# Optimization experiments

Hardware: AMD Instinct MI355X
Metric: run time of the kernel (lower is better)

The kernel has to match this reference:

```python
import jax, jax.numpy as jnp
import numpy as np

N_NODES = 50000
N_EDGES = 800000
D_IN = 128
HIDDEN = 64
N_CLASSES = 2


def gcn_conv(x, edge_index, W, b, num_nodes):
    """PyG GCNConv: linear (no bias) -> add self-loops -> sym-normalized aggregate -> + bias."""
    h = x @ W  # [N, H]
    loop = jnp.arange(num_nodes, dtype=edge_index.dtype)
    src = jnp.concatenate([edge_index[0], loop])  # [E+N]
    dst = jnp.concatenate([edge_index[1], loop])
    deg = jax.ops.segment_sum(jnp.ones_like(dst, dtype=h.dtype), dst, num_segments=num_nodes)
    dinv = jnp.where(deg > 0, jax.lax.rsqrt(deg), 0.0)
    norm = dinv[src] * dinv[dst]  # [E+N]
    msg = h[src] * norm[:, None]  # [E+N, H]  (gather + scale)
    out = jax.ops.segment_sum(msg, dst, num_segments=num_nodes)  # scatter-add
    return out + b


def setup_inputs() -> dict:
    key = jax.random.key(0)
    ks = jax.random.split(key, 6)
    x = jax.random.normal(ks[0], (N_NODES, D_IN), dtype=jnp.float32)
    edge_index = jax.random.randint(ks[1], (2, N_EDGES), 0, N_NODES, dtype=jnp.int64)
    # Glorot-ish init for weights, zero bias (PyG default)
    W1 = jax.random.normal(ks[2], (D_IN, HIDDEN), dtype=jnp.float32) * (1.0 / np.sqrt(D_IN))
    b1 = jnp.zeros((HIDDEN,), dtype=jnp.float32)
    W2 = jax.random.normal(ks[3], (HIDDEN, N_CLASSES), dtype=jnp.float32) * (1.0 / np.sqrt(HIDDEN))
    b2 = jnp.zeros((N_CLASSES,), dtype=jnp.float32)
    return {"x": x, "edge_index": edge_index, "W1": W1, "b1": b1, "W2": W2, "b2": b2}


def reference(x, edge_index, W1, b1, W2, b2):
    h = jax.nn.relu(gcn_conv(x, edge_index, W1, b1, N_NODES))
    # F.dropout(training=self.training) is identity in eval mode
    out = gcn_conv(h, edge_index, W2, b2, N_NODES)
    return out
```

## Files before the change

kernel.cpp:

```cpp
#include <hip/hip_runtime.h>

#define N_NODES 50000
#define N_EDGES 800000
#define D_IN 128
#define HIDDEN 64
#define N_CLASSES 2
#define NBUK 782
#define NBLK 196
#define NE4 200000
#define XPAD 136
#define CAP 2048

typedef _Float16 half4v __attribute__((ext_vector_type(4)));
typedef _Float16 h8 __attribute__((ext_vector_type(8)));
typedef float f4 __attribute__((ext_vector_type(4)));
typedef float f8 __attribute__((ext_vector_type(8)));


__global__ __launch_bounds__(256) void k_gemm_bin(
    const int4* __restrict__ src4, const int4* __restrict__ dst4,
    int* __restrict__ cnt, int* __restrict__ ebin,
    const float* __restrict__ x, const float* __restrict__ W1,
    _Float16* __restrict__ hs)
{
    __shared__ __attribute__((aligned(16))) _Float16 smem[2 * 64 * XPAD];
    const int t = threadIdx.x;

    if (blockIdx.x < NBLK) {
        int* hist = (int*)smem;
        for (int i = t; i < NBUK; i += 256) hist[i] = 0;
        __syncthreads();
        int base4 = blockIdx.x * 1024;
        int4 dv[4], sv[4];
        bool val[4];
#pragma unroll
        for (int k = 0; k < 4; k++) {
            int idx = base4 + k * 256 + t;
            val[k] = (idx < NE4);
            if (val[k]) {
                dv[k] = dst4[idx];
                sv[k] = src4[idx];
                atomicAdd(&hist[dv[k].x >> 6], 1);
                atomicAdd(&hist[dv[k].y >> 6], 1);
                atomicAdd(&hist[dv[k].z >> 6], 1);
                atomicAdd(&hist[dv[k].w >> 6], 1);
            }
        }
        __syncthreads();
        for (int i = t; i < NBUK; i += 256) {
            int c = hist[i];
            hist[i] = c ? atomicAdd(&cnt[i], c) : 0;
        }
        __syncthreads();
#pragma unroll
        for (int k = 0; k < 4; k++) {
            if (val[k]) {
                int b0 = dv[k].x >> 6, b1 = dv[k].y >> 6;
                int b2 = dv[k].z >> 6, b3 = dv[k].w >> 6;
                int p0 = atomicAdd(&hist[b0], 1);
                int p1 = atomicAdd(&hist[b1], 1);
                int p2 = atomicAdd(&hist[b2], 1);
                int p3 = atomicAdd(&hist[b3], 1);
                if (p0 < CAP) ebin[b0 * CAP + p0] = (sv[k].x << 7) | (dv[k].x & 63);
                if (p1 < CAP) ebin[b1 * CAP + p1] = (sv[k].y << 7) | (dv[k].y & 63);
                if (p2 < CAP) ebin[b2 * CAP + p2] = (sv[k].z << 7) | (dv[k].z & 63);
                if (p3 < CAP) ebin[b3 * CAP + p3] = (sv[k].w << 7) | (dv[k].w & 63);
            }
        }
        return;
    }

    _Float16* xs = smem;
    _Float16* Wt = smem + 64 * XPAD;
    const int gb = blockIdx.x - NBLK;
    const int row0 = gb * 64;

    for (int i4 = t; i4 < 64 * D_IN / 4; i4 += 256) {
        int r = i4 >> 5;
        int k4 = (i4 & 31) << 2;
        int grow = row0 + r;
        half4v hv;
        if (grow < N_NODES) {
            float4 v = *(const float4*)&x[grow * D_IN + k4];
            hv.x = (_Float16)v.x; hv.y = (_Float16)v.y;
            hv.z = (_Float16)v.z; hv.w = (_Float16)v.w;
        } else {
            hv.x = hv.y = hv.z = hv.w = (_Float16)0.f;
        }
        *(half4v*)&xs[r * XPAD + k4] = hv;
    }
    for (int i4 = t; i4 < D_IN * HIDDEN / 4; i4 += 256) {
        float4 v = *(const float4*)&W1[i4 * 4];
        int k = i4 >> 4;
        int n = (i4 & 15) << 2;
        Wt[(n + 0) * XPAD + k] = (_Float16)v.x;
        Wt[(n + 1) * XPAD + k] = (_Float16)v.y;
        Wt[(n + 2) * XPAD + k] = (_Float16)v.z;
        Wt[(n + 3) * XPAD + k] = (_Float16)v.w;
    }
    __syncthreads();

    const int w = t >> 6;
    const int L = t & 63;
    const int mrow = w * 16 + (L & 15);
    const int qk = (L >> 4) * 8;
    f4 acc0 = {0.f, 0.f, 0.f, 0.f}, acc1 = acc0, acc2 = acc0, acc3 = acc0;
#pragma unroll
    for (int ks = 0; ks < D_IN; ks += 32) {
        h8 a  = *(const h8*)&xs[mrow * XPAD + ks + qk];
        h8 b0 = *(const h8*)&Wt[(0 * 16 + (L & 15)) * XPAD + ks + qk];
        h8 b1 = *(const h8*)&Wt[(1 * 16 + (L & 15)) * XPAD + ks + qk];
        h8 b2 = *(const h8*)&Wt[(2 * 16 + (L & 15)) * XPAD + ks + qk];
        h8 b3 = *(const h8*)&Wt[(3 * 16 + (L & 15)) * XPAD + ks + qk];
        acc0 = __builtin_amdgcn_mfma_f32_16x16x32_f16(a, b0, acc0, 0, 0, 0);
        acc1 = __builtin_amdgcn_mfma_f32_16x16x32_f16(a, b1, acc1, 0, 0, 0);
        acc2 = __builtin_amdgcn_mfma_f32_16x16x32_f16(a, b2, acc2, 0, 0, 0);
        acc3 = __builtin_amdgcn_mfma_f32_16x16x32_f16(a, b3, acc3, 0, 0, 0);
    }

    const int n0 = L & 15;
#pragma unroll
    for (int j = 0; j < 4; j++) {
        int m = w * 16 + (L >> 4) * 4 + j;
        size_t base = (size_t)(row0 + m) * HIDDEN;
        hs[base + 0 * 16 + n0] = (_Float16)acc0[j];
        hs[base + 1 * 16 + n0] = (_Float16)acc1[j];
        hs[base + 2 * 16 + n0] = (_Float16)acc2[j];
        hs[base + 3 * 16 + n0] = (_Float16)acc3[j];
    }
}


__global__ __launch_bounds__(256) void k_csr_scale(
    const int* __restrict__ ebin, const int* __restrict__ cnt,
    int* __restrict__ rs, int* __restrict__ re, float* __restrict__ dinv_g,
    int* __restrict__ rec, _Float16* __restrict__ hs)
{
    __shared__ int lbin[CAP];
    __shared__ int cnt64[64];
    __shared__ int cur[64];
    __shared__ float sdinv[64];
    const int b = blockIdx.x;
    const int t = threadIdx.x;
    const int row0 = b * 64;
    const int beg = b * CAP;
    const int m = cnt[b];

    if (t < 64) cnt64[t] = 0;
    __syncthreads();
    for (int i = t; i < m; i += 256) {
        int pk = ebin[beg + i];
        lbin[i] = pk;
        atomicAdd(&cnt64[pk & 63], 1);
    }
    __syncthreads();
    if (t < 64) {
        int deg = cnt64[t];
        int sum = deg;
#pragma unroll
        for (int off = 1; off < 64; off <<= 1) {
            int v = __shfl_up(sum, off, 64);
            if (t >= off) sum += v;
        }
        int ex = sum - deg;
        cur[t] = ex;
        float di = rsqrtf((float)(deg + 1));
        sdinv[t] = di;
        int node = row0 + t;
        rs[node] = beg + ex;
        re[node] = beg + ex + deg;
        dinv_g[node] = di;
    }
    __syncthreads();
    for (int i = t; i < m; i += 256) {
        int pk = lbin[i];
        int pos = atomicAdd(&cur[pk & 63], 1);
        rec[beg + pos] = pk >> 7;
    }
    for (int i = t; i < 64 * HIDDEN / 8; i += 256) {
        int r = i >> 3;
        int c = (i & 7) << 3;
        size_t base = (size_t)(row0 + r) * HIDDEN + c;
        h8 hv = *(const h8*)&hs[base];
        float di = sdinv[r];
#pragma unroll
        for (int k = 0; k < 8; k++) hv[k] = (_Float16)((float)hv[k] * di);
        *(h8*)&hs[base] = hv;
    }
}


__global__ __launch_bounds__(256) void k_agg1_l2(
    const _Float16* __restrict__ hs, const int* __restrict__ rs,
    const int* __restrict__ re,
    const int* __restrict__ rec, const float* __restrict__ dinv,
    const float* __restrict__ b1, const float* __restrict__ W2,
    float* __restrict__ zs)
{
    const int node = blockIdx.x * 32 + (threadIdx.x >> 3);
    const int g = threadIdx.x & 7;
    const int gbase = threadIdx.x & 56;
    const h8* H = (const h8*)hs;

    float di = dinv[node];
    f8 acc = {};

    int beg = rs[node];
    int end = re[node];

    int r0 = N_NODES, r1 = N_NODES;
    if (beg < end) {
        int n0 = end - beg; if (n0 > 16) n0 = 16;
        if (2 * g     < n0) r0 = rec[beg + 2 * g];
        if (2 * g + 1 < n0) r1 = rec[beg + 2 * g + 1];
    }

    for (int base = beg; base < end; base += 16) {
        int nb = base + 16;
        int nr0 = N_NODES, nr1 = N_NODES;
        if (nb < end) {
            int nn = end - nb; if (nn > 16) nn = 16;
            if (2 * g     < nn) nr0 = rec[nb + 2 * g];
            if (2 * g + 1 < nn) nr1 = rec[nb + 2 * g + 1];
        }
        int n = end - base;
        if (n > 16) n = 16;
        int n8 = (n + 7) & ~7;
        for (int e = 0; e < n8; e += 8) {
            int q = gbase + (e >> 1);
            int s0 = __shfl(r0, q + 0, 64);
            int s1 = __shfl(r1, q + 0, 64);
            int s2 = __shfl(r0, q + 1, 64);
            int s3 = __shfl(r1, q + 1, 64);
            int s4 = __shfl(r0, q + 2, 64);
            int s5 = __shfl(r1, q + 2, 64);
            int s6 = __shfl(r0, q + 3, 64);
            int s7 = __shfl(r1, q + 3, 64);
            h8 a0 = H[s0 * 8 + g];
            h8 a1 = H[s1 * 8 + g];
            h8 a2 = H[s2 * 8 + g];
            h8 a3 = H[s3 * 8 + g];
            h8 a4 = H[s4 * 8 + g];
            h8 a5 = H[s5 * 8 + g];
            h8 a6 = H[s6 * 8 + g];
            h8 a7 = H[s7 * 8 + g];
#pragma unroll
            for (int k = 0; k < 8; k++) {
                acc[k] += (((float)a0[k] + (float)a1[k]) + ((float)a2[k] + (float)a3[k]))
                        + (((float)a4[k] + (float)a5[k]) + ((float)a6[k] + (float)a7[k]));
            }
        }
        r0 = nr0; r1 = nr1;
    }

    h8 sv = H[node * 8 + g];
#pragma unroll
    for (int k = 0; k < 8; k++) acc[k] += (float)sv[k];

    float4 bbA = ((const float4*)b1)[2 * g];
    float4 bbB = ((const float4*)b1)[2 * g + 1];
    float y[8];
    y[0] = fmaxf(fmaf(acc[0], di, bbA.x), 0.f);
    y[1] = fmaxf(fmaf(acc[1], di, bbA.y), 0.f);
    y[2] = fmaxf(fmaf(acc[2], di, bbA.z), 0.f);
    y[3] = fmaxf(fmaf(acc[3], di, bbA.w), 0.f);
    y[4] = fmaxf(fmaf(acc[4], di, bbB.x), 0.f);
    y[5] = fmaxf(fmaf(acc[5], di, bbB.y), 0.f);
    y[6] = fmaxf(fmaf(acc[6], di, bbB.z), 0.f);
    y[7] = fmaxf(fmaf(acc[7], di, bbB.w), 0.f);
    float p0 = 0.f, p1 = 0.f;
    const float4* W2f4 = (const float4*)W2;
#pragma unroll
    for (int m = 0; m < 4; m++) {
        float4 q = W2f4[4 * g + m];
        p0 += y[2 * m] * q.x + y[2 * m + 1] * q.z;
        p1 += y[2 * m] * q.y + y[2 * m + 1] * q.w;
    }

    p0 += __shfl_down(p0, 4, 64);
    p1 += __shfl_down(p1, 4, 64);
    p0 += __shfl_down(p0, 2, 64);
    p1 += __shfl_down(p1, 2, 64);
    p0 += __shfl_down(p0, 1, 64);
    p1 += __shfl_down(p1, 1, 64);
    if (g == 0) {
        zs[node * 2 + 0] = p0 * di;
        zs[node * 2 + 1] = p1 * di;
    }
}


__global__ __launch_bounds__(256) void k_agg2(
    const float* __restrict__ zs, const int* __restrict__ rs,
    const int* __restrict__ re,
    const int* __restrict__ rec, const float* __restrict__ dinv,
    const float* __restrict__ b2, float* __restrict__ out)
{
    const int node = blockIdx.x * 32 + (threadIdx.x >> 3);
    const int j = threadIdx.x & 7;
    if (node >= N_NODES) return;
    int beg = rs[node];
    int end = re[node];
    float a0 = 0.f, a1 = 0.f;
    int idx = beg + j;
    int s = (idx < end) ? rec[idx] : 0;
    while (idx < end) {
        int nidx = idx + 8;
        int ns = (nidx < end) ? rec[nidx] : 0;
        float2 v = *(const float2*)&zs[s * 2];
        a0 += v.x;
        a1 += v.y;
        idx = nidx;
        s = ns;
    }
    a0 += __shfl_down(a0, 4, 64);
    a1 += __shfl_down(a1, 4, 64);
    a0 += __shfl_down(a0, 2, 64);
    a1 += __shfl_down(a1, 2, 64);
    a0 += __shfl_down(a0, 1, 64);
    a1 += __shfl_down(a1, 1, 64);
    if (j == 0) {
        float di = dinv[node];
        float2 zv = *(const float2*)&zs[node * 2];
        float2 o;
        o.x = fmaf(di, a0 + zv.x, b2[0]);
        o.y = fmaf(di, a1 + zv.y, b2[1]);
        *(float2*)&out[node * 2] = o;
    }
}


extern "C" void kernel_launch(void* const* d_in, const int* in_sizes, int n_in,
                              void* d_out, int out_size, void* d_ws, size_t ws_size,
                              hipStream_t stream) {
    const float* x  = (const float*)d_in[0];
    const int* ei   = (const int*)d_in[1];
    const float* W1 = (const float*)d_in[2];
    const float* b1 = (const float*)d_in[3];
    const float* W2 = (const float*)d_in[4];
    const float* b2 = (const float*)d_in[5];
    float* out = (float*)d_out;

    const int4* src4 = (const int4*)ei;
    const int4* dst4 = (const int4*)(ei + N_EDGES);

    int*      cnt  = (int*)d_ws;
    float*    dinv = (float*)d_ws + 2048;
    int*      rs   = (int*)d_ws + 53248;
    int*      re   = (int*)d_ws + 104448;
    int*      ebin = (int*)d_ws + 155648;
    int*      rec  = (int*)d_ws + 1757184;
    _Float16* hs   = (_Float16*)((int*)d_ws + 3358720);
    float*    zs   = (float*)d_ws + 4960256;

    hipMemsetAsync(cnt, 0, 1024 * sizeof(int), stream);
    k_gemm_bin<<<NBLK + NBUK, 256, 0, stream>>>(src4, dst4, cnt, ebin, x, W1, hs);
    k_csr_scale<<<NBUK, 256, 0, stream>>>(ebin, cnt, rs, re, dinv, rec, hs);
    k_agg1_l2<<<(N_NODES + 31) / 32, 256, 0, stream>>>(hs, rs, re, rec, dinv, b1, W2, zs);
    k_agg2<<<(N_NODES + 31) / 32, 256, 0, stream>>>(zs, rs, re, rec, dinv, b2, out);
}
```

Baseline: 122.8 us.

## Fuse CSR build with layer-1 aggregation using per-edge source dinv weights

After: 129.9 us. 1.06x slower.

```diff
diff --git a/kernel.cpp b/kernel.cpp
--- a/kernel.cpp
+++ b/kernel.cpp
@@ -131,20 +131,43 @@
 }
 
 
-__global__ __launch_bounds__(256) void k_csr_scale(
+__global__ __launch_bounds__(256) void k_dinv(
     const int* __restrict__ ebin, const int* __restrict__ cnt,
-    int* __restrict__ rs, int* __restrict__ re, float* __restrict__ dinv_g,
-    int* __restrict__ rec, _Float16* __restrict__ hs)
+    float* __restrict__ dinv_g)
+{
+    __shared__ int cnt64[64];
+    const int b = blockIdx.x;
+    const int t = threadIdx.x;
+    const int beg = b * CAP;
+    int m = cnt[b]; if (m > CAP) m = CAP;
+
+    if (t < 64) cnt64[t] = 0;
+    __syncthreads();
+    for (int i = t; i < m; i += 256) atomicAdd(&cnt64[ebin[beg + i] & 63], 1);
+    __syncthreads();
+    if (t < 64) dinv_g[b * 64 + t] = rsqrtf((float)(cnt64[t] + 1));
+}
+
+
+__global__ __launch_bounds__(256) void k_csr_agg1(
+    const int* __restrict__ ebin, const int* __restrict__ cnt,
+    const float* __restrict__ dinv, const _Float16* __restrict__ hs,
+    const float* __restrict__ b1, const float* __restrict__ W2,
+    int* __restrict__ rs, int* __restrict__ re, int* __restrict__ rec,
+    float* __restrict__ zs)
 {
     __shared__ int lbin[CAP];
+    __shared__ int lrec[CAP];
+    __shared__ float ldin[CAP];
     __shared__ int cnt64[64];
-    __shared__ int cur[64];
+    __shared__ int cur64[64];
+    __shared__ int lst[64];
     __shared__ float sdinv[64];
     const int b = blockIdx.x;
     const int t = threadIdx.x;
     const int row0 = b * 64;
     const int beg = b * CAP;
-    const int m = cnt[b];
+    int m = cnt[b]; if (m > CAP) m = CAP;
 
     if (t < 64) cnt64[t] = 0;
     __syncthreads();
@@ -163,122 +186,90 @@
             if (t >= off) sum += v;
         }
         int ex = sum - deg;
-        cur[t] = ex;
-        float di = rsqrtf((float)(deg + 1));
-        sdinv[t] = di;
+        cur64[t] = ex;
+        lst[t] = ex;
+        sdinv[t] = rsqrtf((float)(deg + 1));
         int node = row0 + t;
         rs[node] = beg + ex;
         re[node] = beg + ex + deg;
-        dinv_g[node] = di;
     }
     __syncthreads();
     for (int i = t; i < m; i += 256) {
         int pk = lbin[i];
-        int pos = atomicAdd(&cur[pk & 63], 1);
-        rec[beg + pos] = pk >> 7;
-    }
-    for (int i = t; i < 64 * HIDDEN / 8; i += 256) {
-        int r = i >> 3;
-        int c = (i & 7) << 3;
-        size_t base = (size_t)(row0 + r) * HIDDEN + c;
-        h8 hv = *(const h8*)&hs[base];
-        float di = sdinv[r];
-#pragma unroll
-        for (int k = 0; k < 8; k++) hv[k] = (_Float16)((float)hv[k] * di);
-        *(h8*)&hs[base] = hv;
-    }
-}
-
-
-__global__ __launch_bounds__(256) void k_agg1_l2(
-    const _Float16* __restrict__ hs, const int* __restrict__ rs,
-    const int* __restrict__ re,
-    const int* __restrict__ rec, const float* __restrict__ dinv,
-    const float* __restrict__ b1, const float* __restrict__ W2,
-    float* __restrict__ zs)
-{
-    const int node = blockIdx.x * 32 + (threadIdx.x >> 3);
-    const int g = threadIdx.x & 7;
-    const int gbase = threadIdx.x & 56;
+        int src = pk >> 7;
+        int pos = atomicAdd(&cur64[pk & 63], 1);
+        lrec[pos] = src;
+        ldin[pos] = dinv[src];
+        rec[beg + pos] = src;
+    }
+    __syncthreads();
+
+    const int nl = t >> 2;
+    const int g = t & 3;
+    const int node = row0 + nl;
+    const int ls = lst[nl];
+    const int deg = cnt64[nl];
+    const float di = sdinv[nl];
     const h8* H = (const h8*)hs;
-
-    float di = dinv[node];
-    f8 acc = {};
-
-    int beg = rs[node];
-    int end = re[node];
-
-    int r0 = N_NODES, r1 = N_NODES;
-    if (beg < end) {
-        int n0 = end - beg; if (n0 > 16) n0 = 16;
-        if (2 * g     < n0) r0 = rec[beg + 2 * g];
-        if (2 * g + 1 < n0) r1 = rec[beg + 2 * g + 1];
-    }
-
-    for (int base = beg; base < end; base += 16) {
-        int nb = base + 16;
-        int nr0 = N_NODES, nr1 = N_NODES;
-        if (nb < end) {
-            int nn = end - nb; if (nn > 16) nn = 16;
-            if (2 * g     < nn) nr0 = rec[nb + 2 * g];
-            if (2 * g + 1 < nn) nr1 = rec[nb + 2 * g + 1];
-        }
-        int n = end - base;
-        if (n > 16) n = 16;
-        int n8 = (n + 7) & ~7;
-        for (int e = 0; e < n8; e += 8) {
-            int q = gbase + (e >> 1);
-            int s0 = __shfl(r0, q + 0, 64);
-            int s1 = __shfl(r1, q + 0, 64);
-            int s2 = __shfl(r0, q + 1, 64);
-            int s3 = __shfl(r1, q + 1, 64);
-            int s4 = __shfl(r0, q + 2, 64);
-            int s5 = __shfl(r1, q + 2, 64);
-            int s6 = __shfl(r0, q + 3, 64);
-            int s7 = __shfl(r1, q + 3, 64);
-            h8 a0 = H[s0 * 8 + g];
-            h8 a1 = H[s1 * 8 + g];
-            h8 a2 = H[s2 * 8 + g];
-            h8 a3 = H[s3 * 8 + g];
-            h8 a4 = H[s4 * 8 + g];
-            h8 a5 = H[s5 * 8 + g];
-            h8 a6 = H[s6 * 8 + g];
-            h8 a7 = H[s7 * 8 + g];
-#pragma unroll
-            for (int k = 0; k < 8; k++) {
-                acc[k] += (((float)a0[k] + (float)a1[k]) + ((float)a2[k] + (float)a3[k]))
-                        + (((float)a4[k] + (float)a5[k]) + ((float)a6[k] + (float)a7[k]));
-            }
-        }
-        r0 = nr0; r1 = nr1;
-    }
-
-    h8 sv = H[node * 8 + g];
-#pragma unroll
-    for (int k = 0; k < 8; k++) acc[k] += (float)sv[k];
-
-    float4 bbA = ((const float4*)b1)[2 * g];
-    float4 bbB = ((const float4*)b1)[2 * g + 1];
-    float y[8];
-    y[0] = fmaxf(fmaf(acc[0], di, bbA.x), 0.f);
-    y[1] = fmaxf(fmaf(acc[1], di, bbA.y), 0.f);
-    y[2] = fmaxf(fmaf(acc[2], di, bbA.z), 0.f);
-    y[3] = fmaxf(fmaf(acc[3], di, bbA.w), 0.f);
-    y[4] = fmaxf(fmaf(acc[4], di, bbB.x), 0.f);
-    y[5] = fmaxf(fmaf(acc[5], di, bbB.y), 0.f);
-    y[6] = fmaxf(fmaf(acc[6], di, bbB.z), 0.f);
-    y[7] = fmaxf(fmaf(acc[7], di, bbB.w), 0.f);
+    f8 accA = {}, accB = {};
+
+    for (int e = 0; e < deg; e += 4) {
+        int s0 = lrec[ls + e];                      float f0 = ldin[ls + e];
+        int s1 = N_NODES, s2 = N_NODES, s3 = N_NODES;
+        float f1 = 0.f, f2 = 0.f, f3 = 0.f;
+        if (e + 1 < deg) { s1 = lrec[ls + e + 1]; f1 = ldin[ls + e + 1]; }
+        if (e + 2 < deg) { s2 = lrec[ls + e + 2]; f2 = ldin[ls + e + 2]; }
+        if (e + 3 < deg) { s3 = lrec[ls + e + 3]; f3 = ldin[ls + e + 3]; }
+        h8 a0 = H[s0 * 8 + 2 * g], c0 = H[s0 * 8 + 2 * g + 1];
+        h8 a1 = H[s1 * 8 + 2 * g], c1 = H[s1 * 8 + 2 * g + 1];
+        h8 a2 = H[s2 * 8 + 2 * g], c2 = H[s2 * 8 + 2 * g + 1];
+        h8 a3 = H[s3 * 8 + 2 * g], c3 = H[s3 * 8 + 2 * g + 1];
+#pragma unroll
+        for (int k = 0; k < 8; k++) {
+            accA[k] += f0 * (float)a0[k] + f1 * (float)a1[k]
+                     + f2 * (float)a2[k] + f3 * (float)a3[k];
+            accB[k] += f0 * (float)c0[k] + f1 * (float)c1[k]
+                     + f2 * (float)c2[k] + f3 * (float)c3[k];
+        }
+    }
+
+    h8 sA = H[node * 8 + 2 * g], sB = H[node * 8 + 2 * g + 1];
+#pragma unroll
+    for (int k = 0; k < 8; k++) {
+        accA[k] += di * (float)sA[k];
+        accB[k] += di * (float)sB[k];
+    }
+
+    const float4* B1 = (const float4*)b1;
+    float4 q0 = B1[4 * g + 0], q1 = B1[4 * g + 1];
+    float4 q2 = B1[4 * g + 2], q3 = B1[4 * g + 3];
+    float y[16];
+    y[0]  = fmaxf(fmaf(accA[0], di, q0.x), 0.f);
+    y[1]  = fmaxf(fmaf(accA[1], di, q0.y), 0.f);
+    y[2]  = fmaxf(fmaf(accA[2], di, q0.z), 0.f);
+    y[3]  = fmaxf(fmaf(accA[3], di, q0.w), 0.f);
+    y[4]  = fmaxf(fmaf(accA[4], di, q1.x), 0.f);
+    y[5]  = fmaxf(fmaf(accA[5], di, q1.y), 0.f);
+    y[6]  = fmaxf(fmaf(accA[6], di, q1.z), 0.f);
+    y[7]  = fmaxf(fmaf(accA[7], di, q1.w), 0.f);
+    y[8]  = fmaxf(fmaf(accB[0], di, q2.x), 0.f);
+    y[9]  = fmaxf(fmaf(accB[1], di, q2.y), 0.f);
+    y[10] = fmaxf(fmaf(accB[2], di, q2.z), 0.f);
+    y[11] = fmaxf(fmaf(accB[3], di, q2.w), 0.f);
+    y[12] = fmaxf(fmaf(accB[4], di, q3.x), 0.f);
+    y[13] = fmaxf(fmaf(accB[5], di, q3.y), 0.f);
+    y[14] = fmaxf(fmaf(accB[6], di, q3.z), 0.f);
+    y[15] = fmaxf(fmaf(accB[7], di, q3.w), 0.f);
+
     float p0 = 0.f, p1 = 0.f;
     const float4* W2f4 = (const float4*)W2;
 #pragma unroll
-    for (int m = 0; m < 4; m++) {
-        float4 q = W2f4[4 * g + m];
-        p0 += y[2 * m] * q.x + y[2 * m + 1] * q.z;
-        p1 += y[2 * m] * q.y + y[2 * m + 1] * q.w;
-    }
-
-    p0 += __shfl_down(p0, 4, 64);
-    p1 += __shfl_down(p1, 4, 64);
+    for (int r = 0; r < 8; r++) {
+        float4 q = W2f4[8 * g + r];
+        p0 += y[2 * r] * q.x + y[2 * r + 1] * q.z;
+        p1 += y[2 * r] * q.y + y[2 * r + 1] * q.w;
+    }
+
     p0 += __shfl_down(p0, 2, 64);
     p1 += __shfl_down(p1, 2, 64);
     p0 += __shfl_down(p0, 1, 64);
@@ -355,7 +346,7 @@
 
     hipMemsetAsync(cnt, 0, 1024 * sizeof(int), stream);
     k_gemm_bin<<<NBLK + NBUK, 256, 0, stream>>>(src4, dst4, cnt, ebin, x, W1, hs);
-    k_csr_scale<<<NBUK, 256, 0, stream>>>(ebin, cnt, rs, re, dinv, rec, hs);
-    k_agg1_l2<<<(N_NODES + 31) / 32, 256, 0, stream>>>(hs, rs, re, rec, dinv, b1, W2, zs);
+    k_dinv<<<NBUK, 256, 0, stream>>>(ebin, cnt, dinv);
+    k_csr_agg1<<<NBUK, 256, 0, stream>>>(ebin, cnt, dinv, hs, b1, W2, rs, re, rec, zs);
     k_agg2<<<(N_NODES + 31) / 32, 256, 0, stream>>>(zs, rs, re, rec, dinv, b2, out);
 }
```
